# Optimization experiments

Measured on AMD Instinct MI355X. Metric: run time of the kernel, lower is better.

## Reference

```python
import jax, jax.numpy as jnp
import numpy as np

EPS = 1e-5  # torch default eps for both LayerNorm and BatchNorm
NH, KD, HD = 8, 16, 32  # num_heads, key_dim, head_dim for inc=256


def conv1x1(x, w, b=None):
    # w: [Cout, Cin]; x: [B, Cin, H, W]
    y = jnp.einsum('oc,bchw->bohw', w, x)
    return y if b is None else y + b[None, :, None, None]


def dwconv3x3(x, w, b=None):
    # depthwise 3x3, padding 1; w: [C, 1, 3, 3]
    C = x.shape[1]
    y = jax.lax.conv_general_dilated(x, w, (1, 1), ((1, 1), (1, 1)),
                                     dimension_numbers=('NCHW', 'OIHW', 'NCHW'),
                                     feature_group_count=C)
    return y if b is None else y + b[None, :, None, None]


def bn_eval(x, p):
    # p: [4, C] stacked (gamma, beta, running_mean, running_var); eval-mode BN
    g, b, m, v = p
    s = (g * jax.lax.rsqrt(v + EPS))[None, :, None, None]
    return (x - m[None, :, None, None]) * s + b[None, :, None, None]


def ln2d(x, g, b):
    # LayerNorm over channel dim (== permute->LN(C)->permute in torch)
    mu = x.mean(axis=1, keepdims=True)
    var = x.var(axis=1, keepdims=True)  # biased var, matches F.layer_norm
    return (x - mu) * jax.lax.rsqrt(var + EPS) * g[None, :, None, None] + b[None, :, None, None]


def setup_inputs() -> dict:
    key = jax.random.key(0)
    ks = jax.random.split(key, 20)
    B, C, H, W = 8, 256, 32, 32
    h_qkv = C + 2 * NH * KD  # 512
    hid = int(2 * C / 3)     # 170

    def bn_params(k, c):
        k1, k2, k3, k4 = jax.random.split(k, 4)
        g = 1.0 + 0.1 * jax.random.normal(k1, (c,), jnp.float32)
        b = 0.1 * jax.random.normal(k2, (c,), jnp.float32)
        m = 0.1 * jax.random.normal(k3, (c,), jnp.float32)
        v = jax.random.uniform(k4, (c,), jnp.float32, 0.5, 1.5)
        return jnp.stack([g, b, m, v])

    sc = lambda fan: 1.0 / np.sqrt(fan)
    return {
        'x': jax.random.normal(ks[0], (B, C, H, W), jnp.float32),
        'ln1_g': 1.0 + 0.1 * jax.random.normal(ks[1], (C,), jnp.float32),
        'ln1_b': 0.1 * jax.random.normal(ks[2], (C,), jnp.float32),
        'ln2_g': 1.0 + 0.1 * jax.random.normal(ks[3], (C,), jnp.float32),
        'ln2_b': 0.1 * jax.random.normal(ks[4], (C,), jnp.float32),
        'qkv_w': sc(C) * jax.random.normal(ks[5], (h_qkv, C), jnp.float32),
        'qkv_bn': bn_params(ks[6], h_qkv),
        'pe_w': sc(9) * jax.random.normal(ks[7], (C, 1, 3, 3), jnp.float32),
        'pe_bn': bn_params(ks[8], C),
        'proj_w': sc(C) * jax.random.normal(ks[9], (C, C), jnp.float32),
        'proj_bn': bn_params(ks[10], C),
        'fc1_w': sc(C) * jax.random.normal(ks[11], (2 * hid, C), jnp.float32),
        'fc1_b': 0.01 * jax.random.normal(ks[12], (2 * hid,), jnp.float32),
        'dw_w': sc(9) * jax.random.normal(ks[13], (hid, 1, 3, 3), jnp.float32),
        'dw_b': 0.01 * jax.random.normal(ks[14], (hid,), jnp.float32),
        'fc2_w': sc(hid) * jax.random.normal(ks[15], (C, hid), jnp.float32),
        'fc2_b': 0.01 * jax.random.normal(ks[16], (C,), jnp.float32),
    }


def reference(x, ln1_g, ln1_b, ln2_g, ln2_b, qkv_w, qkv_bn, pe_w, pe_bn,
              proj_w, proj_bn, fc1_w, fc1_b, dw_w, dw_b, fc2_w, fc2_b):
    B, C, H, W = x.shape
    N = H * W

    # --- PSA attention branch (eval mode: drop_path = identity) ---
    xn = ln2d(x, ln1_g, ln1_b)
    qkv = bn_eval(conv1x1(xn, qkv_w), qkv_bn)            # [B, 2*nh*kd + C, H, W]
    qkv = qkv.reshape(B, NH, 2 * KD + HD, N)
    q, k, v = qkv[:, :, :KD], qkv[:, :, KD:2 * KD], qkv[:, :, 2 * KD:]
    scale = KD ** -0.5
    attn = jax.nn.softmax(jnp.einsum('bhkn,bhkm->bhnm', q, k) * scale, axis=-1)
    o = jnp.einsum('bhdm,bhnm->bhdn', v, attn).reshape(B, C, H, W)
    o = o + bn_eval(dwconv3x3(v.reshape(B, C, H, W), pe_w), pe_bn)
    o = bn_eval(conv1x1(o, proj_w), proj_bn)
    x = x + o

    # --- Convolutional GLU branch (internal residual uses normed input) ---
    xn2 = ln2d(x, ln2_g, ln2_b)
    h = conv1x1(xn2, fc1_w, fc1_b)
    a, g = jnp.split(h, 2, axis=1)
    a = jax.nn.gelu(dwconv3x3(a, dw_w, dw_b), approximate=False) * g
    mlp_out = xn2 + conv1x1(a, fc2_w, fc2_b)
    return x + mlp_out
```

## Files before the change

### kernel.cpp

```cpp
#include <hip/hip_runtime.h>
#include <hip/hip_bf16.h>
#include <math.h>

#define EPSF 1e-5f

using short2v = __attribute__((ext_vector_type(2))) short;
using short4v = __attribute__((ext_vector_type(4))) short;
using short8 = __attribute__((ext_vector_type(8))) short;
using f32x4 = __attribute__((ext_vector_type(4))) float;

__device__ inline short bfbits(float x) {
  __hip_bfloat16 h = __float2bfloat16(x);
  return __builtin_bit_cast(short, h);
}
__device__ inline float bf2f(short s) {
  unsigned u = ((unsigned)(unsigned short)s) << 16;
  return __builtin_bit_cast(float, u);
}

__global__ __launch_bounds__(256) void prep_kernel(
    const float* __restrict__ qkv_w, const float* __restrict__ qkv_bn,
    const float* __restrict__ proj_w, const float* __restrict__ proj_bn,
    const float* __restrict__ fc1_w, const float* __restrict__ fc2_w,
    const float* __restrict__ pe_w, const float* __restrict__ pe_bn,
    const float* __restrict__ dw_w, const float* __restrict__ dw_b,
    short* __restrict__ wq, float* __restrict__ bq, short* __restrict__ wpj,
    float* __restrict__ bpj, short* __restrict__ wf1, short* __restrict__ wf2,
    float* __restrict__ pwT, float* __restrict__ pbv, float* __restrict__ wdT,
    float* __restrict__ dbv) {
  int id = blockIdx.x * 256 + threadIdx.x;
  if (id < 131072) {
    int o = id >> 8, k = id & 255;
    float g = qkv_bn[o], bb = qkv_bn[512 + o], m = qkv_bn[1024 + o],
          v = qkv_bn[1536 + o];
    float s = g * rsqrtf(v + EPSF);
    float s2 = ((o & 63) < 16) ? 0.25f * 1.44269504088896f : 1.0f;
    wq[id] = bfbits(qkv_w[id] * s * s2);
    if (k == 0) bq[o] = (bb - m * s) * s2;
  } else if (id < 196608) {
    int i = id - 131072;
    int o = i >> 8, k = i & 255;
    float g = proj_bn[o], bb = proj_bn[256 + o], m = proj_bn[512 + o],
          v = proj_bn[768 + o];
    float s = g * rsqrtf(v + EPSF);
    wpj[i] = bfbits(proj_w[i] * s);
    if (k == 0) bpj[o] = bb - m * s;
  } else if (id < 294912) {
    int i = id - 196608;
    int o = i >> 8, k = i & 255;
    wf1[i] = bfbits(o < 340 ? fc1_w[o * 256 + k] : 0.f);
  } else if (id < 344064) {
    int i = id - 294912;
    int o = i / 192, k = i - o * 192;
    wf2[i] = bfbits(k < 170 ? fc2_w[o * 170 + k] : 0.f);
  } else if (id < 346368) {
    int i = id - 344064;
    int c = i & 255, tap = i >> 8;
    float g = pe_bn[c], bb = pe_bn[256 + c], m = pe_bn[512 + c],
          v = pe_bn[768 + c];
    float s = g * rsqrtf(v + EPSF);
    pwT[tap * 256 + c] = pe_w[c * 9 + tap] * s;
    if (tap == 0) pbv[c] = bb - m * s;
  } else if (id < 348096) {
    int i = id - 346368;
    int c = i % 192, tap = i / 192;
    wdT[tap * 192 + c] = (c < 170) ? dw_w[c * 9 + tap] : 0.f;
    if (tap == 0) dbv[c] = (c < 170) ? dw_b[c] : 0.f;
  }
}

__global__ __launch_bounds__(256) void ln1_kernel(
    const float* __restrict__ x, const float* __restrict__ gamma,
    const float* __restrict__ beta, short* __restrict__ xn) {
  __shared__ float s_sum[16][16];
  __shared__ float s_sq[16][16];
  int t = threadIdx.x;
  int nl = t & 15, cg = t >> 4;
  int p0 = blockIdx.x * 16;
  int b = p0 >> 10;
  int n = (p0 & 1023) + nl;
  const float* xp = x + ((size_t)b * 256 + cg * 16) * 1024 + n;
  float v[16];
  float sum = 0.f, sq = 0.f;
#pragma unroll
  for (int i = 0; i < 16; ++i) {
    float val = xp[(size_t)i * 1024];
    v[i] = val;
    sum += val;
    sq += val * val;
  }
  s_sum[cg][nl] = sum;
  s_sq[cg][nl] = sq;
  __syncthreads();
  float ts = 0.f, tq = 0.f;
#pragma unroll
  for (int g = 0; g < 16; ++g) {
    ts += s_sum[g][nl];
    tq += s_sq[g][nl];
  }
  float mu = ts * (1.f / 256.f);
  float var = tq * (1.f / 256.f) - mu * mu;
  float rs = rsqrtf(var + EPSF);
  short8 pk[2];
#pragma unroll
  for (int i = 0; i < 16; ++i) {
    int c = cg * 16 + i;
    pk[i >> 3][i & 7] = bfbits((v[i] - mu) * rs * gamma[c] + beta[c]);
  }
  short* op = xn + ((size_t)b * 1024 + n) * 256 + cg * 16;
  *reinterpret_cast<short8*>(op) = pk[0];
  *reinterpret_cast<short8*>(op + 8) = pk[1];
}

__global__ __launch_bounds__(256) void ln2_kernel(
    const float* __restrict__ x1, const float* __restrict__ gamma,
    const float* __restrict__ beta, short* __restrict__ xn2) {
  int t = threadIdx.x;
  int lane = t & 63, w = t >> 6;
  f32x4 gv = *reinterpret_cast<const f32x4*>(&gamma[lane * 4]);
  f32x4 bv = *reinterpret_cast<const f32x4*>(&beta[lane * 4]);
#pragma unroll
  for (int it = 0; it < 4; ++it) {
    size_t pos = blockIdx.x * 16 + w * 4 + it;
    f32x4 xv = *reinterpret_cast<const f32x4*>(&x1[pos * 256 + lane * 4]);
    float s = (xv[0] + xv[1]) + (xv[2] + xv[3]);
    float q = (xv[0] * xv[0] + xv[1] * xv[1]) + (xv[2] * xv[2] + xv[3] * xv[3]);
#pragma unroll
    for (int off = 1; off < 64; off <<= 1) {
      s += __shfl_xor(s, off);
      q += __shfl_xor(q, off);
    }
    float mu = s * (1.f / 256.f);
    float var = q * (1.f / 256.f) - mu * mu;
    float rs = rsqrtf(var + EPSF);
    short4v o;
#pragma unroll
    for (int e = 0; e < 4; ++e)
      o[e] = bfbits((xv[e] - mu) * rs * gv[e] + bv[e]);
    *reinterpret_cast<short4v*>(&xn2[pos * 256 + lane * 4]) = o;
  }
}

template <int MODE>
__global__ __launch_bounds__(256) void gemm4_kernel(
    const short* __restrict__ X, const short* __restrict__ W,
    const float* __restrict__ bias, const float* __restrict__ addCM,
    const float* __restrict__ add1CL, const short* __restrict__ add2CL,
    void* __restrict__ out, int OC, int K, int OT, int KS, int RS) {
  __shared__ short Wl[128][72];
  __shared__ short Xl[64][72];
  int bx = blockIdx.x;
  int ot = bx % OT;
  int ntb = bx / OT;
  int b = ntb >> 4;
  int n0 = (ntb & 15) * 64;
  int o0 = ot * 128;
  int t = threadIdx.x;
  int lane = t & 63, w = t >> 6;
  int wo = w >> 1, wn = w & 1;
  int g = lane >> 4, r = lane & 15;
  int rw = t >> 1, cw = (t & 1) * 32;
  int rx = t >> 2, cx = (t & 3) * 16;
  size_t bN = (size_t)b * 1024;
  const short* Wp = W + (size_t)(o0 + rw) * K + cw;
  const short* Xp = X + (bN + n0 + rx) * KS + cx;
  f32x4 acc[4][2] = {};
  int nsteps = K >> 6;
  short8 wreg[4], xreg[2];
#pragma unroll
  for (int e = 0; e < 4; ++e)
    wreg[e] = *reinterpret_cast<const short8*>(Wp + e * 8);
#pragma unroll
  for (int e = 0; e < 2; ++e)
    xreg[e] = *reinterpret_cast<const short8*>(Xp + e * 8);
  for (int ks = 0; ks < nsteps; ++ks) {
#pragma unroll
    for (int e = 0; e < 4; ++e)
      *reinterpret_cast<short8*>(&Wl[rw][cw + e * 8]) = wreg[e];
#pragma unroll
    for (int e = 0; e < 2; ++e)
      *reinterpret_cast<short8*>(&Xl[rx][cx + e * 8]) = xreg[e];
    __syncthreads();
    if (ks + 1 < nsteps) {
      int ko = (ks + 1) << 6;
#pragma unroll
      for (int e = 0; e < 4; ++e)
        wreg[e] = *reinterpret_cast<const short8*>(Wp + ko + e * 8);
#pragma unroll
      for (int e = 0; e < 2; ++e)
        xreg[e] = *reinterpret_cast<const short8*>(Xp + ko + e * 8);
    }
#pragma unroll
    for (int kk = 0; kk < 2; ++kk) {
      short8 a[4], bb[2];
#pragma unroll
      for (int i = 0; i < 4; ++i)
        a[i] = *reinterpret_cast<const short8*>(
            &Wl[wo * 64 + i * 16 + r][kk * 32 + g * 8]);
#pragma unroll
      for (int j = 0; j < 2; ++j)
        bb[j] = *reinterpret_cast<const short8*>(
            &Xl[wn * 32 + j * 16 + r][kk * 32 + g * 8]);
#pragma unroll
      for (int i = 0; i < 4; ++i)
#pragma unroll
        for (int j = 0; j < 2; ++j)
          acc[i][j] = __builtin_amdgcn_mfma_f32_16x16x32_bf16(
              a[i], bb[j], acc[i][j], 0, 0, 0);
    }
    __syncthreads();
  }
#pragma unroll
  for (int i = 0; i < 4; ++i) {
#pragma unroll
    for (int j = 0; j < 2; ++j) {
      int oq = o0 + wo * 64 + i * 16 + g * 4;
      if (oq >= OC) continue;
      int n = n0 + wn * 32 + j * 16 + r;
      f32x4 bv = *reinterpret_cast<const f32x4*>(&bias[oq]);
      f32x4 res;
#pragma unroll
      for (int rr = 0; rr < 4; ++rr) res[rr] = acc[i][j][rr] + bv[rr];
      if constexpr (MODE == 0) {
        short4v s;
#pragma unroll
        for (int rr = 0; rr < 4; ++rr) s[rr] = bfbits(res[rr]);
        *reinterpret_cast<short4v*>((short*)out + (bN + n) * RS + oq) = s;
      } else if constexpr (MODE == 1) {
#pragma unroll
        for (int rr = 0; rr < 4; ++rr)
          res[rr] += addCM[((size_t)b * 256 + oq + rr) * 1024 + n];
        *reinterpret_cast<f32x4*>((float*)out + (bN + n) * 256 + oq) = res;
      } else {
        f32x4 a1v = *reinterpret_cast<const f32x4*>(&add1CL[(bN + n) * 256 + oq]);
        short4v a2v = *reinterpret_cast<const short4v*>(&add2CL[(bN + n) * 256 + oq]);
#pragma unroll
        for (int rr = 0; rr < 4; ++rr) {
          float v = res[rr] + a1v[rr] + bf2f(a2v[rr]);
          ((float*)out)[((size_t)b * 256 + oq + rr) * 1024 + n] = v;
        }
      }
    }
  }
}

__global__ __launch_bounds__(256) void attn4_kernel(
    const short* __restrict__ qkv, const float* __restrict__ pwT,
    const float* __restrict__ pbv, short* __restrict__ obf) {
  __shared__ short Ql[64][40];
  __shared__ short Kl[2][64][40];
  __shared__ short Vl[2][32][72];
  __shared__ short Ol[64][36];
  int blk = blockIdx.x;
  int h = blk & 7, qt = (blk >> 3) & 15, b = blk >> 7;
  size_t bN = (size_t)b * 1024;
  const short* base = qkv + bN * 512 + h * 64;
  int t = threadIdx.x;
  int lane = t & 63, w = t >> 6;
  int g = lane >> 4, r = lane & 15;
  int q0 = qt * 64;
  for (int i = t; i < 64 * 16; i += 256) {
    int row = i >> 4, col = 16 + (i & 15);
    Ql[row][col] = 0;
    Kl[0][row][col] = 0;
    Kl[1][row][col] = 0;
  }
  {
    int qr = t >> 2, kd4 = (t & 3) * 4;
    short4v qv =
        *reinterpret_cast<const short4v*>(&base[(size_t)(q0 + qr) * 512 + kd4]);
    *reinterpret_cast<short4v*>(&Ql[qr][kd4]) = qv;
  }
  int mr4 = t >> 2, kd4 = (t & 3) * 4;
  int mp = t & 31, dq8 = t >> 5;
  short4v kreg =
      *reinterpret_cast<const short4v*>(&base[(size_t)mr4 * 512 + 16 + kd4]);
  short4v vA = *reinterpret_cast<const short4v*>(
      &base[(size_t)(2 * mp) * 512 + 32 + dq8 * 4]);
  short4v vB = *reinterpret_cast<const short4v*>(
      &base[(size_t)(2 * mp + 1) * 512 + 32 + dq8 * 4]);
  *reinterpret_cast<short4v*>(&Kl[0][mr4][kd4]) = kreg;
#pragma unroll
  for (int e = 0; e < 4; ++e) {
    short2v p = {vA[e], vB[e]};
    *reinterpret_cast<short2v*>(&Vl[0][dq8 * 4 + e][2 * mp]) = p;
  }
  __syncthreads();
  short8 qf = *reinterpret_cast<const short8*>(&Ql[w * 16 + r][g * 8]);
  float M = -3e38f, l = 0.f;
  f32x4 O0 = {}, O1 = {};
  for (int ch = 0; ch < 16; ++ch) {
    int cur = ch & 1;
    if (ch + 1 < 16) {
      int m0 = (ch + 1) * 64;
      kreg = *reinterpret_cast<const short4v*>(
          &base[(size_t)(m0 + mr4) * 512 + 16 + kd4]);
      vA = *reinterpret_cast<const short4v*>(
          &base[(size_t)(m0 + 2 * mp) * 512 + 32 + dq8 * 4]);
      vB = *reinterpret_cast<const short4v*>(
          &base[(size_t)(m0 + 2 * mp + 1) * 512 + 32 + dq8 * 4]);
    }
    f32x4 s4[4];
#pragma unroll
    for (int mt = 0; mt < 4; ++mt) {
      short8 af = *reinterpret_cast<const short8*>(&Kl[cur][mt * 16 + r][g * 8]);
      f32x4 z = {};
      s4[mt] = __builtin_amdgcn_mfma_f32_16x16x32_bf16(af, qf, z, 0, 0, 0);
    }
    float pm = -3e38f;
#pragma unroll
    for (int mt = 0; mt < 4; ++mt)
      pm = fmaxf(pm,
                 fmaxf(fmaxf(s4[mt][0], s4[mt][1]), fmaxf(s4[mt][2], s4[mt][3])));
    pm = fmaxf(pm, __shfl_xor(pm, 16));
    pm = fmaxf(pm, __shfl_xor(pm, 32));
    bool full = !__all(pm - M <= 8.f);
    float Mn = full ? fmaxf(M, pm) : M;
    float f = full ? exp2f(M - Mn) : 1.f;
    M = Mn;
    float sc = 0.f;
    short8 pa[4];
#pragma unroll
    for (int mt = 0; mt < 4; ++mt) {
      float p0 = exp2f(s4[mt][0] - Mn);
      float p1 = exp2f(s4[mt][1] - Mn);
      float p2 = exp2f(s4[mt][2] - Mn);
      float p3 = exp2f(s4[mt][3] - Mn);
      sc += (p0 + p1) + (p2 + p3);
      pa[mt] = (short8){bfbits(p0), bfbits(p1), bfbits(p2), bfbits(p3),
                        0, 0, 0, 0};
    }
    sc += __shfl_xor(sc, 16);
    sc += __shfl_xor(sc, 32);
    l = l * f + sc;
    if (full) {
#pragma unroll
      for (int rr = 0; rr < 4; ++rr) {
        float fr = __shfl(f, g * 4 + rr);
        O0[rr] *= fr;
        O1[rr] *= fr;
      }
    }
#pragma unroll
    for (int mt = 0; mt < 4; ++mt) {
      short4v v0 = *reinterpret_cast<const short4v*>(&Vl[cur][r][mt * 16 + g * 4]);
      short4v v1 =
          *reinterpret_cast<const short4v*>(&Vl[cur][16 + r][mt * 16 + g * 4]);
      short8 b0 = {v0[0], v0[1], v0[2], v0[3], 0, 0, 0, 0};
      short8 b1 = {v1[0], v1[1], v1[2], v1[3], 0, 0, 0, 0};
      O0 = __builtin_amdgcn_mfma_f32_16x16x32_bf16(pa[mt], b0, O0, 0, 0, 0);
      O1 = __builtin_amdgcn_mfma_f32_16x16x32_bf16(pa[mt], b1, O1, 0, 0, 0);
    }
    if (ch + 1 < 16) {
      int nxt = cur ^ 1;
      *reinterpret_cast<short4v*>(&Kl[nxt][mr4][kd4]) = kreg;
#pragma unroll
      for (int e = 0; e < 4; ++e) {
        short2v p = {vA[e], vB[e]};
        *reinterpret_cast<short2v*>(&Vl[nxt][dq8 * 4 + e][2 * mp]) = p;
      }
    }
    __syncthreads();
  }
#pragma unroll
  for (int rr = 0; rr < 4; ++rr) {
    float lr = __shfl(l, g * 4 + rr);
    float inv = 1.f / lr;
    int q = w * 16 + g * 4 + rr;
    Ol[q][r] = bfbits(O0[rr] * inv);
    Ol[q][16 + r] = bfbits(O1[rr] * inv);
  }
  __syncthreads();
#pragma unroll
  for (int it = 0; it < 2; ++it) {
    int item = t + it * 256;
    int q = item & 63, dq = item >> 6;
    int n = q0 + q;
    int y = n >> 5, xx = n & 31;
    int cq = h * 32 + dq * 4;
    f32x4 s = *reinterpret_cast<const f32x4*>(&pbv[cq]);
#pragma unroll
    for (int dy = -1; dy <= 1; ++dy) {
      int yy = y + dy;
      if (yy < 0 || yy > 31) continue;
#pragma unroll
      for (int dx = -1; dx <= 1; ++dx) {
        int xw = xx + dx;
        if (xw < 0 || xw > 31) continue;
        int tap = (dy + 1) * 3 + (dx + 1);
        f32x4 wv = *reinterpret_cast<const f32x4*>(&pwT[tap * 256 + cq]);
        short4v vv = *reinterpret_cast<const short4v*>(
            &base[(size_t)(yy * 32 + xw) * 512 + 32 + dq * 4]);
#pragma unroll
        for (int e = 0; e < 4; ++e) s[e] += wv[e] * bf2f(vv[e]);
      }
    }
    short4v ov = *reinterpret_cast<const short4v*>(&Ol[q][dq * 4]);
    short4v res;
#pragma unroll
    for (int e = 0; e < 4; ++e) res[e] = bfbits(bf2f(ov[e]) + s[e]);
    *reinterpret_cast<short4v*>(&obf[(bN + n) * 256 + cq]) = res;
  }
}

__global__ __launch_bounds__(256) void glu3_kernel(
    const short* __restrict__ h, const float* __restrict__ wdT,
    const float* __restrict__ dbv, short* __restrict__ act) {
  int t = threadIdx.x;
  int pos = blockIdx.x * 16 + (t >> 4);
  int c0 = (t & 15) * 12;
  int n = pos & 1023;
  int b = pos >> 10;
  int y = n >> 5, xx = n & 31;
  const short* hb = h + (size_t)b * 1024 * 352;
  float s[12];
#pragma unroll
  for (int e = 0; e < 12; ++e) s[e] = dbv[c0 + e];
#pragma unroll
  for (int dy = -1; dy <= 1; ++dy) {
    int yy = y + dy;
    if (yy < 0 || yy > 31) continue;
#pragma unroll
    for (int dx = -1; dx <= 1; ++dx) {
      int xw = xx + dx;
      if (xw < 0 || xw > 31) continue;
      int tap = (dy + 1) * 3 + (dx + 1);
      const float* wp = wdT + tap * 192 + c0;
      const short* ap = hb + (size_t)(yy * 32 + xw) * 352 + c0;
#pragma unroll
      for (int v4 = 0; v4 < 3; ++v4) {
        short4v av = *reinterpret_cast<const short4v*>(ap + v4 * 4);
        f32x4 wv = *reinterpret_cast<const f32x4*>(wp + v4 * 4);
#pragma unroll
        for (int e = 0; e < 4; ++e) s[v4 * 4 + e] += wv[e] * bf2f(av[e]);
      }
    }
  }
  const short* gp = hb + (size_t)n * 352 + 170 + c0;
  short* arow = act + ((size_t)b * 1024 + n) * 192 + c0;
#pragma unroll
  for (int v4 = 0; v4 < 3; ++v4) {
    short4v res;
#pragma unroll
    for (int e = 0; e < 4; ++e) {
      float sv = s[v4 * 4 + e];
      float ge = 0.5f * sv * (1.f + erff(sv * 0.70710678118654752f));
      res[e] = bfbits(ge * bf2f(gp[v4 * 4 + e]));
    }
    *reinterpret_cast<short4v*>(arow + v4 * 4) = res;
  }
}

extern "C" void kernel_launch(void* const* d_in, const int* in_sizes, int n_in,
                              void* d_out, int out_size, void* d_ws,
                              size_t ws_size, hipStream_t stream) {
  const float* x      = (const float*)d_in[0];
  const float* ln1_g  = (const float*)d_in[1];
  const float* ln1_b  = (const float*)d_in[2];
  const float* ln2_g  = (const float*)d_in[3];
  const float* ln2_b  = (const float*)d_in[4];
  const float* qkv_w  = (const float*)d_in[5];
  const float* qkv_bn = (const float*)d_in[6];
  const float* pe_w   = (const float*)d_in[7];
  const float* pe_bn  = (const float*)d_in[8];
  const float* proj_w = (const float*)d_in[9];
  const float* proj_bn= (const float*)d_in[10];
  const float* fc1_w  = (const float*)d_in[11];
  const float* fc1_b  = (const float*)d_in[12];
  const float* dw_w   = (const float*)d_in[13];
  const float* dw_b   = (const float*)d_in[14];
  const float* fc2_w  = (const float*)d_in[15];
  const float* fc2_b  = (const float*)d_in[16];

  char* base = (char*)d_ws;
  short* xn   = (short*)(base + 0);
  short* qkv  = (short*)(base + 4194304);
  short* obf  = (short*)(base + 12582912);
  float* x1   = (float*)(base + 16777216);
  short* xn2  = (short*)(base + 25165824);
  short* hbuf = (short*)(base + 29360128);
  short* act  = (short*)(base + 35131392);
  short* wq   = (short*)(base + 38277120);
  short* wpj  = (short*)(base + 38539264);
  short* wf1  = (short*)(base + 38670336);
  short* wf2  = (short*)(base + 38866944);
  float* pwT  = (float*)(base + 38965248);
  float* pbv  = (float*)(base + 38974464);
  float* wdT  = (float*)(base + 38975488);
  float* dbv  = (float*)(base + 38982400);
  float* bq   = (float*)(base + 38983168);
  float* bpj  = (float*)(base + 38985216);
  float* outp = (float*)d_out;

  hipLaunchKernelGGL(prep_kernel, dim3(1360), dim3(256), 0, stream, qkv_w,
                     qkv_bn, proj_w, proj_bn, fc1_w, fc2_w, pe_w, pe_bn, dw_w,
                     dw_b, wq, bq, wpj, bpj, wf1, wf2, pwT, pbv, wdT, dbv);
  hipLaunchKernelGGL(ln1_kernel, dim3(512), dim3(256), 0, stream, x, ln1_g,
                     ln1_b, xn);
  hipLaunchKernelGGL((gemm4_kernel<0>), dim3(512), dim3(256), 0, stream, xn,
                     wq, bq, nullptr, nullptr, nullptr, qkv, 512, 256, 4, 256,
                     512);
  hipLaunchKernelGGL(attn4_kernel, dim3(1024), dim3(256), 0, stream, qkv, pwT,
                     pbv, obf);
  hipLaunchKernelGGL((gemm4_kernel<1>), dim3(256), dim3(256), 0, stream, obf,
                     wpj, bpj, x, nullptr, nullptr, x1, 256, 256, 2, 256, 256);
  hipLaunchKernelGGL(ln2_kernel, dim3(512), dim3(256), 0, stream, x1, ln2_g,
                     ln2_b, xn2);
  hipLaunchKernelGGL((gemm4_kernel<0>), dim3(384), dim3(256), 0, stream, xn2,
                     wf1, fc1_b, nullptr, nullptr, nullptr, hbuf, 340, 256, 3,
                     256, 352);
  hipLaunchKernelGGL(glu3_kernel, dim3(512), dim3(256), 0, stream, hbuf, wdT,
                     dbv, act);
  hipLaunchKernelGGL((gemm4_kernel<2>), dim3(256), dim3(256), 0, stream, act,
                     wf2, fc2_b, nullptr, x1, xn2, outp, 256, 192, 2, 192,
                     256);
}
```

Measured before the change: 177.6 us.

## Emit transposed V from QKV GEMM and double attention key chunk size

```diff
diff --git a/kernel.cpp b/kernel.cpp
--- a/kernel.cpp
+++ b/kernel.cpp
@@ -142,11 +142,12 @@
 }
 
 template <int MODE>
-__global__ __launch_bounds__(256) void gemm4_kernel(
+__global__ __launch_bounds__(256) void gemm6_kernel(
     const short* __restrict__ X, const short* __restrict__ W,
     const float* __restrict__ bias, const float* __restrict__ addCM,
     const float* __restrict__ add1CL, const short* __restrict__ add2CL,
-    void* __restrict__ out, int OC, int K, int OT, int KS, int RS) {
+    void* __restrict__ out, short* __restrict__ vTout, int OC, int K, int OT,
+    int KS, int RS) {
   __shared__ short Wl[128][72];
   __shared__ short Xl[64][72];
   int bx = blockIdx.x;
@@ -221,11 +222,22 @@
       f32x4 res;
 #pragma unroll
       for (int rr = 0; rr < 4; ++rr) res[rr] = acc[i][j][rr] + bv[rr];
-      if constexpr (MODE == 0) {
+      if constexpr (MODE == 0 || MODE == 3) {
         short4v s;
 #pragma unroll
         for (int rr = 0; rr < 4; ++rr) s[rr] = bfbits(res[rr]);
         *reinterpret_cast<short4v*>((short*)out + (bN + n) * RS + oq) = s;
+        if constexpr (MODE == 3) {
+          int sub = oq & 63;
+          if (sub >= 32) {
+            int head = oq >> 6, d = sub - 32;
+            size_t vb = ((size_t)(b * 8 + head) * 32 + d) * 1024 + n;
+            vTout[vb] = s[0];
+            vTout[vb + 1024] = s[1];
+            vTout[vb + 2048] = s[2];
+            vTout[vb + 3072] = s[3];
+          }
+        }
       } else if constexpr (MODE == 1) {
 #pragma unroll
         for (int rr = 0; rr < 4; ++rr)
@@ -244,123 +256,109 @@
   }
 }
 
-__global__ __launch_bounds__(256) void attn4_kernel(
-    const short* __restrict__ qkv, const float* __restrict__ pwT,
-    const float* __restrict__ pbv, short* __restrict__ obf) {
-  __shared__ short Ql[64][40];
-  __shared__ short Kl[2][64][40];
-  __shared__ short Vl[2][32][72];
+__global__ __launch_bounds__(256) void attn6_kernel(
+    const short* __restrict__ qkv, const short* __restrict__ vT,
+    const float* __restrict__ pwT, const float* __restrict__ pbv,
+    short* __restrict__ obf) {
+  __shared__ short Kl[2][128][24];
+  __shared__ short Vl[2][32][136];
   __shared__ short Ol[64][36];
   int blk = blockIdx.x;
   int h = blk & 7, qt = (blk >> 3) & 15, b = blk >> 7;
   size_t bN = (size_t)b * 1024;
   const short* base = qkv + bN * 512 + h * 64;
+  const short* vTb = vT + (size_t)(b * 8 + h) * 32 * 1024;
   int t = threadIdx.x;
   int lane = t & 63, w = t >> 6;
   int g = lane >> 4, r = lane & 15;
   int q0 = qt * 64;
-  for (int i = t; i < 64 * 16; i += 256) {
-    int row = i >> 4, col = 16 + (i & 15);
-    Ql[row][col] = 0;
-    Kl[0][row][col] = 0;
-    Kl[1][row][col] = 0;
-  }
-  {
-    int qr = t >> 2, kd4 = (t & 3) * 4;
-    short4v qv =
-        *reinterpret_cast<const short4v*>(&base[(size_t)(q0 + qr) * 512 + kd4]);
-    *reinterpret_cast<short4v*>(&Ql[qr][kd4]) = qv;
-  }
-  int mr4 = t >> 2, kd4 = (t & 3) * 4;
-  int mp = t & 31, dq8 = t >> 5;
-  short4v kreg =
-      *reinterpret_cast<const short4v*>(&base[(size_t)mr4 * 512 + 16 + kd4]);
-  short4v vA = *reinterpret_cast<const short4v*>(
-      &base[(size_t)(2 * mp) * 512 + 32 + dq8 * 4]);
-  short4v vB = *reinterpret_cast<const short4v*>(
-      &base[(size_t)(2 * mp + 1) * 512 + 32 + dq8 * 4]);
-  *reinterpret_cast<short4v*>(&Kl[0][mr4][kd4]) = kreg;
-#pragma unroll
-  for (int e = 0; e < 4; ++e) {
-    short2v p = {vA[e], vB[e]};
-    *reinterpret_cast<short2v*>(&Vl[0][dq8 * 4 + e][2 * mp]) = p;
-  }
-  __syncthreads();
-  short8 qf = *reinterpret_cast<const short8*>(&Ql[w * 16 + r][g * 8]);
+  short8 qf = {};
+  if (g < 2)
+    qf = *reinterpret_cast<const short8*>(
+        &base[(size_t)(q0 + w * 16 + r) * 512 + g * 8]);
+  int km = t >> 1, kh = (t & 1) * 8;
+  int vd = t >> 3, vm = (t & 7) * 16;
+  short8 kreg =
+      *reinterpret_cast<const short8*>(&base[(size_t)km * 512 + 16 + kh]);
+  short8 vreg0 = *reinterpret_cast<const short8*>(&vTb[(size_t)vd * 1024 + vm]);
+  short8 vreg1 =
+      *reinterpret_cast<const short8*>(&vTb[(size_t)vd * 1024 + vm + 8]);
   float M = -3e38f, l = 0.f;
   f32x4 O0 = {}, O1 = {};
-  for (int ch = 0; ch < 16; ++ch) {
+  for (int ch = 0; ch < 8; ++ch) {
     int cur = ch & 1;
-    if (ch + 1 < 16) {
-      int m0 = (ch + 1) * 64;
-      kreg = *reinterpret_cast<const short4v*>(
-          &base[(size_t)(m0 + mr4) * 512 + 16 + kd4]);
-      vA = *reinterpret_cast<const short4v*>(
-          &base[(size_t)(m0 + 2 * mp) * 512 + 32 + dq8 * 4]);
-      vB = *reinterpret_cast<const short4v*>(
-          &base[(size_t)(m0 + 2 * mp + 1) * 512 + 32 + dq8 * 4]);
-    }
-    f32x4 s4[4];
-#pragma unroll
-    for (int mt = 0; mt < 4; ++mt) {
-      short8 af = *reinterpret_cast<const short8*>(&Kl[cur][mt * 16 + r][g * 8]);
-      f32x4 z = {};
-      s4[mt] = __builtin_amdgcn_mfma_f32_16x16x32_bf16(af, qf, z, 0, 0, 0);
-    }
-    float pm = -3e38f;
-#pragma unroll
-    for (int mt = 0; mt < 4; ++mt)
-      pm = fmaxf(pm,
-                 fmaxf(fmaxf(s4[mt][0], s4[mt][1]), fmaxf(s4[mt][2], s4[mt][3])));
-    pm = fmaxf(pm, __shfl_xor(pm, 16));
-    pm = fmaxf(pm, __shfl_xor(pm, 32));
-    bool full = !__all(pm - M <= 8.f);
-    float Mn = full ? fmaxf(M, pm) : M;
-    float f = full ? exp2f(M - Mn) : 1.f;
-    M = Mn;
-    float sc = 0.f;
-    short8 pa[4];
-#pragma unroll
-    for (int mt = 0; mt < 4; ++mt) {
-      float p0 = exp2f(s4[mt][0] - Mn);
-      float p1 = exp2f(s4[mt][1] - Mn);
-      float p2 = exp2f(s4[mt][2] - Mn);
-      float p3 = exp2f(s4[mt][3] - Mn);
-      sc += (p0 + p1) + (p2 + p3);
-      pa[mt] = (short8){bfbits(p0), bfbits(p1), bfbits(p2), bfbits(p3),
-                        0, 0, 0, 0};
-    }
-    sc += __shfl_xor(sc, 16);
-    sc += __shfl_xor(sc, 32);
-    l = l * f + sc;
-    if (full) {
-#pragma unroll
-      for (int rr = 0; rr < 4; ++rr) {
-        float fr = __shfl(f, g * 4 + rr);
-        O0[rr] *= fr;
-        O1[rr] *= fr;
-      }
-    }
-#pragma unroll
-    for (int mt = 0; mt < 4; ++mt) {
-      short4v v0 = *reinterpret_cast<const short4v*>(&Vl[cur][r][mt * 16 + g * 4]);
-      short4v v1 =
-          *reinterpret_cast<const short4v*>(&Vl[cur][16 + r][mt * 16 + g * 4]);
-      short8 b0 = {v0[0], v0[1], v0[2], v0[3], 0, 0, 0, 0};
-      short8 b1 = {v1[0], v1[1], v1[2], v1[3], 0, 0, 0, 0};
-      O0 = __builtin_amdgcn_mfma_f32_16x16x32_bf16(pa[mt], b0, O0, 0, 0, 0);
-      O1 = __builtin_amdgcn_mfma_f32_16x16x32_bf16(pa[mt], b1, O1, 0, 0, 0);
-    }
-    if (ch + 1 < 16) {
-      int nxt = cur ^ 1;
-      *reinterpret_cast<short4v*>(&Kl[nxt][mr4][kd4]) = kreg;
-#pragma unroll
-      for (int e = 0; e < 4; ++e) {
-        short2v p = {vA[e], vB[e]};
-        *reinterpret_cast<short2v*>(&Vl[nxt][dq8 * 4 + e][2 * mp]) = p;
-      }
-    }
+    *reinterpret_cast<short8*>(&Kl[cur][km][kh]) = kreg;
+    *reinterpret_cast<short8*>(&Vl[cur][vd][vm]) = vreg0;
+    *reinterpret_cast<short8*>(&Vl[cur][vd][vm + 8]) = vreg1;
     __syncthreads();
+    if (ch + 1 < 8) {
+      int m0 = (ch + 1) * 128;
+      kreg = *reinterpret_cast<const short8*>(
+          &base[(size_t)(m0 + km) * 512 + 16 + kh]);
+      vreg0 =
+          *reinterpret_cast<const short8*>(&vTb[(size_t)vd * 1024 + m0 + vm]);
+      vreg1 = *reinterpret_cast<const short8*>(
+          &vTb[(size_t)vd * 1024 + m0 + vm + 8]);
+    }
+#pragma unroll
+    for (int sub = 0; sub < 2; ++sub) {
+      int mb = sub * 64;
+      f32x4 s4[4];
+#pragma unroll
+      for (int mt = 0; mt < 4; ++mt) {
+        short8 af = {};
+        if (g < 2)
+          af = *reinterpret_cast<const short8*>(
+              &Kl[cur][mb + mt * 16 + r][g * 8]);
+        f32x4 z = {};
+        s4[mt] = __builtin_amdgcn_mfma_f32_16x16x32_bf16(af, qf, z, 0, 0, 0);
+      }
+      float pm = -3e38f;
+#pragma unroll
+      for (int mt = 0; mt < 4; ++mt)
+        pm = fmaxf(pm, fmaxf(fmaxf(s4[mt][0], s4[mt][1]),
+                             fmaxf(s4[mt][2], s4[mt][3])));
+      pm = fmaxf(pm, __shfl_xor(pm, 16));
+      pm = fmaxf(pm, __shfl_xor(pm, 32));
+      bool full = !__all(pm - M <= 8.f);
+      float Mn = full ? fmaxf(M, pm) : M;
+      float f = full ? exp2f(M - Mn) : 1.f;
+      M = Mn;
+      float sc = 0.f;
+      short8 pa[4];
+#pragma unroll
+      for (int mt = 0; mt < 4; ++mt) {
+        float p0 = exp2f(s4[mt][0] - Mn);
+        float p1 = exp2f(s4[mt][1] - Mn);
+        float p2 = exp2f(s4[mt][2] - Mn);
+        float p3 = exp2f(s4[mt][3] - Mn);
+        sc += (p0 + p1) + (p2 + p3);
+        pa[mt] = (short8){bfbits(p0), bfbits(p1), bfbits(p2), bfbits(p3),
+                          0, 0, 0, 0};
+      }
+      sc += __shfl_xor(sc, 16);
+      sc += __shfl_xor(sc, 32);
+      l = l * f + sc;
+      if (full) {
+#pragma unroll
+        for (int rr = 0; rr < 4; ++rr) {
+          float fr = __shfl(f, g * 4 + rr);
+          O0[rr] *= fr;
+          O1[rr] *= fr;
+        }
+      }
+#pragma unroll
+      for (int mt = 0; mt < 4; ++mt) {
+        short4v v0 = *reinterpret_cast<const short4v*>(
+            &Vl[cur][r][mb + mt * 16 + g * 4]);
+        short4v v1 = *reinterpret_cast<const short4v*>(
+            &Vl[cur][16 + r][mb + mt * 16 + g * 4]);
+        short8 b0 = {v0[0], v0[1], v0[2], v0[3], 0, 0, 0, 0};
+        short8 b1 = {v1[0], v1[1], v1[2], v1[3], 0, 0, 0, 0};
+        O0 = __builtin_amdgcn_mfma_f32_16x16x32_bf16(pa[mt], b0, O0, 0, 0, 0);
+        O1 = __builtin_amdgcn_mfma_f32_16x16x32_bf16(pa[mt], b1, O1, 0, 0, 0);
+      }
+    }
   }
 #pragma unroll
   for (int rr = 0; rr < 4; ++rr) {
@@ -490,6 +488,7 @@
   float* dbv  = (float*)(base + 38982400);
   float* bq   = (float*)(base + 38983168);
   float* bpj  = (float*)(base + 38985216);
+  short* vT   = (short*)(base + 40894464);
   float* outp = (float*)d_out;
 
   hipLaunchKernelGGL(prep_kernel, dim3(1360), dim3(256), 0, stream, qkv_w,
@@ -497,21 +496,22 @@
                      dw_b, wq, bq, wpj, bpj, wf1, wf2, pwT, pbv, wdT, dbv);
   hipLaunchKernelGGL(ln1_kernel, dim3(512), dim3(256), 0, stream, x, ln1_g,
                      ln1_b, xn);
-  hipLaunchKernelGGL((gemm4_kernel<0>), dim3(512), dim3(256), 0, stream, xn,
-                     wq, bq, nullptr, nullptr, nullptr, qkv, 512, 256, 4, 256,
-                     512);
-  hipLaunchKernelGGL(attn4_kernel, dim3(1024), dim3(256), 0, stream, qkv, pwT,
-                     pbv, obf);
-  hipLaunchKernelGGL((gemm4_kernel<1>), dim3(256), dim3(256), 0, stream, obf,
-                     wpj, bpj, x, nullptr, nullptr, x1, 256, 256, 2, 256, 256);
+  hipLaunchKernelGGL((gemm6_kernel<3>), dim3(512), dim3(256), 0, stream, xn,
+                     wq, bq, nullptr, nullptr, nullptr, qkv, vT, 512, 256, 4,
+                     256, 512);
+  hipLaunchKernelGGL(attn6_kernel, dim3(1024), dim3(256), 0, stream, qkv, vT,
+                     pwT, pbv, obf);
+  hipLaunchKernelGGL((gemm6_kernel<1>), dim3(256), dim3(256), 0, stream, obf,
+                     wpj, bpj, x, nullptr, nullptr, x1, nullptr, 256, 256, 2,
+                     256, 256);
   hipLaunchKernelGGL(ln2_kernel, dim3(512), dim3(256), 0, stream, x1, ln2_g,
                      ln2_b, xn2);
-  hipLaunchKernelGGL((gemm4_kernel<0>), dim3(384), dim3(256), 0, stream, xn2,
-                     wf1, fc1_b, nullptr, nullptr, nullptr, hbuf, 340, 256, 3,
-                     256, 352);
+  hipLaunchKernelGGL((gemm6_kernel<0>), dim3(384), dim3(256), 0, stream, xn2,
+                     wf1, fc1_b, nullptr, nullptr, nullptr, hbuf, nullptr, 340,
+                     256, 3, 256, 352);
   hipLaunchKernelGGL(glu3_kernel, dim3(512), dim3(256), 0, stream, hbuf, wdT,
                      dbv, act);
-  hipLaunchKernelGGL((gemm4_kernel<2>), dim3(256), dim3(256), 0, stream, act,
-                     wf2, fc2_b, nullptr, x1, xn2, outp, 256, 192, 2, 192,
-                     256);
-}
+  hipLaunchKernelGGL((gemm6_kernel<2>), dim3(256), dim3(256), 0, stream, act,
+                     wf2, fc2_b, nullptr, x1, xn2, outp, nullptr, 256, 192, 2,
+                     192, 256);
+}
```

New measurement: 179.5 us. No clear change (+1.1%).
